# Optimization experiments

Measured on AMD Instinct MI355X. Metric: run time of the kernel, lower is better.

Reference implementation:

```python
import jax, jax.numpy as jnp
import numpy as np
import math

LOCAL_WINDOW = 256  # matches init_kwargs local_window

B, H, S, DK = 1, 16, 2048, 64


def setup_inputs() -> dict:
    key = jax.random.key(0)
    kq, kk, kv = jax.random.split(key, 3)
    return {
        "q": jax.random.normal(kq, (B, H, S, DK), dtype=jnp.float32),
        "k": jax.random.normal(kk, (B, H, S, DK), dtype=jnp.float32),
        "v": jax.random.normal(kv, (B, H, S, DK), dtype=jnp.float32),
        "layer_idx": 1,
        "training": 0,
    }


def _make_mask(seq_len: int, layer_idx: int) -> jnp.ndarray:
    i = jnp.arange(seq_len)[:, None]
    j = jnp.arange(seq_len)[None, :]
    causal = j <= i
    if layer_idx % 2 == 0:
        return causal  # full causal mask
    # local banded mask: causal AND within local_window
    return causal & ((i - j) < LOCAL_WINDOW)


def reference(q, k, v, layer_idx, training):
    # past=None path: no KV-cache concat; present = (k, v)
    dk = q.shape[-1]
    # scores: [B, H, S, S]
    scores = jnp.einsum("bhqd,bhkd->bhqk", q, k) / math.sqrt(dk)
    seq_len = scores.shape[-1]
    mask = _make_mask(seq_len, layer_idx)  # [S, S], broadcast over B, H
    scores = jnp.where(mask, scores, jnp.float32(-1e9))
    weights = jax.nn.softmax(scores, axis=-1)
    # training=0 -> no dropout (deterministic reference)
    context = jnp.einsum("bhqk,bhkd->bhqd", weights, v)
    return (context, k, v)  # (context, present)
```

## Files before the change

### kernel.cpp

```cpp
#include <hip/hip_runtime.h>

#define S_DIM 2048
#define H_DIM 16
#define DK_DIM 64
#define TQ 64
#define TK 64
#define KSP 72
#define VTP 72
#define PSP 72
#define WINDOW 256

typedef short short8 __attribute__((ext_vector_type(8)));
typedef float floatx4 __attribute__((ext_vector_type(4)));

static __device__ __forceinline__ short f2bf(float f) {
    unsigned u = __builtin_bit_cast(unsigned, f);
    u = (u + 0x7fffu + ((u >> 16) & 1u)) >> 16;
    return (short)u;
}

__global__ __launch_bounds__(256, 2)
void attn_kernel(const float* __restrict__ qg,
                 const float* __restrict__ kg,
                 const float* __restrict__ vg,
                 const int* __restrict__ layer_idx_p,
                 float* __restrict__ outc,
                 float* __restrict__ outk,
                 float* __restrict__ outv)
{
    __shared__ __align__(16) short Ks[TK * KSP];
    __shared__ __align__(16) short Vts[DK_DIM * VTP];
    __shared__ __align__(16) short Ps[4 * 16 * PSP];

    const int bid  = blockIdx.x;
    const int h    = bid >> 5;
    const int q0   = (bid & 31) * TQ;
    const int tid  = threadIdx.x;
    const int w    = tid >> 6;
    const int lane = tid & 63;
    const int quad = lane >> 4;
    const int l16  = lane & 15;

    const int li  = layer_idx_p[0];
    const int wnd = (li & 1) ? WINDOW : S_DIM;

    {
        const size_t base = ((size_t)(h * S_DIM + q0)) * DK_DIM;
        const floatx4* ks4 = (const floatx4*)(kg + base);
        const floatx4* vs4 = (const floatx4*)(vg + base);
        floatx4* ok4 = (floatx4*)(outk + base);
        floatx4* ov4 = (floatx4*)(outv + base);
        #pragma unroll
        for (int i = 0; i < 4; ++i) {
            int f = tid + i * 256;
            ok4[f] = ks4[f];
            ov4[f] = vs4[f];
        }
    }

    const int qrow = q0 + w * 16 + l16;
    const size_t qbase = ((size_t)(h * S_DIM + qrow)) * DK_DIM;
    short8 qf0, qf1;
    {
        floatx4 a0 = *(const floatx4*)(qg + qbase + quad * 8);
        floatx4 a1 = *(const floatx4*)(qg + qbase + quad * 8 + 4);
        floatx4 b0 = *(const floatx4*)(qg + qbase + 32 + quad * 8);
        floatx4 b1 = *(const floatx4*)(qg + qbase + 32 + quad * 8 + 4);
        #pragma unroll
        for (int j = 0; j < 4; ++j) {
            qf0[j]     = f2bf(a0[j] * 0.125f);
            qf0[j + 4] = f2bf(a1[j] * 0.125f);
            qf1[j]     = f2bf(b0[j] * 0.125f);
            qf1[j + 4] = f2bf(b1[j] * 0.125f);
        }
    }

    floatx4 Oacc[4];
    floatx4 Lacc = (floatx4){0.f, 0.f, 0.f, 0.f};
    #pragma unroll
    for (int dt = 0; dt < 4; ++dt) Oacc[dt] = (floatx4){0.f, 0.f, 0.f, 0.f};

    short8 ones;
    #pragma unroll
    for (int j = 0; j < 8; ++j) ones[j] = (short)0x3F80;

    int lo = q0 - (wnd - 1); if (lo < 0) lo = 0;
    const int kb0  = lo & ~(TK - 1);
    const int kend = q0 + TQ - 1;

    floatx4 kraw[2][2];
    float   vraw[2][8];
    const int krow[2] = { (tid * 8) >> 6, ((tid + 256) * 8) >> 6 };
    const int kcol[2] = { (tid * 8) & 63, ((tid + 256) * 8) & 63 };
    const int vd  [2] = { tid & 63, (tid + 256) & 63 };
    const int vkg [2] = { tid >> 6, (tid + 256) >> 6 };

    auto preload = [&](int kb) {
        #pragma unroll
        for (int it = 0; it < 2; ++it) {
            const float* p = kg + ((size_t)(h * S_DIM + kb + krow[it])) * DK_DIM + kcol[it];
            kraw[it][0] = *(const floatx4*)p;
            kraw[it][1] = *(const floatx4*)(p + 4);
            #pragma unroll
            for (int j = 0; j < 8; ++j)
                vraw[it][j] = vg[((size_t)(h * S_DIM + kb + vkg[it] * 8 + j)) * DK_DIM + vd[it]];
        }
    };
    auto commit = [&]() {
        #pragma unroll
        for (int it = 0; it < 2; ++it) {
            short8 val;
            #pragma unroll
            for (int j = 0; j < 4; ++j) {
                val[j]     = f2bf(kraw[it][0][j]);
                val[j + 4] = f2bf(kraw[it][1][j]);
            }
            *(short8*)(&Ks[krow[it] * KSP + kcol[it]]) = val;
            short8 tmp;
            #pragma unroll
            for (int j = 0; j < 8; ++j) tmp[j] = f2bf(vraw[it][j]);
            *(short8*)(&Vts[vd[it] * VTP + vkg[it] * 8]) = tmp;
        }
    };

    preload(kb0);

    for (int kb = kb0; kb <= kend; kb += TK) {
        commit();
        __syncthreads();
        if (kb + TK <= kend) preload(kb + TK);

        #pragma unroll
        for (int ct = 0; ct < 4; ++ct) {
            floatx4 acc = (floatx4){0.f, 0.f, 0.f, 0.f};
            short8 b0 = *(const short8*)(&Ks[(ct * 16 + l16) * KSP +      quad * 8]);
            acc = __builtin_amdgcn_mfma_f32_16x16x32_bf16(qf0, b0, acc, 0, 0, 0);
            short8 b1 = *(const short8*)(&Ks[(ct * 16 + l16) * KSP + 32 + quad * 8]);
            acc = __builtin_amdgcn_mfma_f32_16x16x32_bf16(qf1, b1, acc, 0, 0, 0);
            const int col = kb + ct * 16 + l16;
            #pragma unroll
            for (int r = 0; r < 4; ++r) {
                int row = q0 + w * 16 + quad * 4 + r;
                bool valid = (col <= row) && ((row - col) < wnd);
                float pv = valid ? __expf(acc[r]) : 0.f;
                Ps[(w * 16 + quad * 4 + r) * PSP + ct * 16 + l16] = f2bf(pv);
            }
        }

        #pragma unroll
        for (int ks = 0; ks < 2; ++ks) {
            short8 af = *(const short8*)(&Ps[(w * 16 + l16) * PSP + ks * 32 + quad * 8]);
            Lacc = __builtin_amdgcn_mfma_f32_16x16x32_bf16(af, ones, Lacc, 0, 0, 0);
            #pragma unroll
            for (int dt = 0; dt < 4; ++dt) {
                short8 bf = *(const short8*)(&Vts[(dt * 16 + l16) * VTP + ks * 32 + quad * 8]);
                Oacc[dt] = __builtin_amdgcn_mfma_f32_16x16x32_bf16(af, bf, Oacc[dt], 0, 0, 0);
            }
        }
        __syncthreads();
    }

    #pragma unroll
    for (int r = 0; r < 4; ++r) {
        float inv = 1.0f / Lacc[r];
        int row = q0 + w * 16 + quad * 4 + r;
        size_t obase = ((size_t)(h * S_DIM + row)) * DK_DIM;
        #pragma unroll
        for (int dt = 0; dt < 4; ++dt)
            outc[obase + dt * 16 + l16] = Oacc[dt][r] * inv;
    }
}

extern "C" void kernel_launch(void* const* d_in, const int* in_sizes, int n_in,
                              void* d_out, int out_size, void* d_ws, size_t ws_size,
                              hipStream_t stream) {
    const float* q  = (const float*)d_in[0];
    const float* k  = (const float*)d_in[1];
    const float* v  = (const float*)d_in[2];
    const int* li   = (const int*)d_in[3];
    float* out      = (float*)d_out;

    const int nctx = in_sizes[0];
    float* outk = out + nctx;
    float* outv = out + nctx + in_sizes[1];

    const int grid_attn = H_DIM * (S_DIM / TQ);
    attn_kernel<<<grid_attn, 256, 0, stream>>>(q, k, v, li, out, outk, outv);
}
```

Before: 97.29 us.

## Halve query tile and split key tiles across two wave groups

Measured after the change: 120.2 us. +23.6%, slower.

```diff
diff --git a/kernel.cpp b/kernel.cpp
--- a/kernel.cpp
+++ b/kernel.cpp
@@ -3,11 +3,9 @@
 #define S_DIM 2048
 #define H_DIM 16
 #define DK_DIM 64
-#define TQ 64
+#define TQ 32
 #define TK 64
-#define KSP 72
-#define VTP 72
-#define PSP 72
+#define PST 70
 #define WINDOW 256
 
 typedef short short8 __attribute__((ext_vector_type(8)));
@@ -19,7 +17,7 @@
     return (short)u;
 }
 
-__global__ __launch_bounds__(256, 2)
+__global__ __launch_bounds__(256, 3)
 void attn_kernel(const float* __restrict__ qg,
                  const float* __restrict__ kg,
                  const float* __restrict__ vg,
@@ -28,18 +26,21 @@
                  float* __restrict__ outk,
                  float* __restrict__ outv)
 {
-    __shared__ __align__(16) short Ks[TK * KSP];
-    __shared__ __align__(16) short Vts[DK_DIM * VTP];
-    __shared__ __align__(16) short Ps[4 * 16 * PSP];
+    __shared__ __align__(16) short Kst[2][TK * PST];
+    __shared__ __align__(16) short Vst[2][DK_DIM * PST];
+    __shared__ __align__(16) short Ps[4][16 * PST];
 
     const int bid  = blockIdx.x;
-    const int h    = bid >> 5;
-    const int q0   = (bid & 31) * TQ;
+    const int h    = bid >> 6;
+    const int q0   = (bid & 63) * TQ;
     const int tid  = threadIdx.x;
     const int w    = tid >> 6;
     const int lane = tid & 63;
     const int quad = lane >> 4;
     const int l16  = lane & 15;
+    const int qsub = w & 1;
+    const int kgrp = w >> 1;
+    const int t128 = tid & 127;
 
     const int li  = layer_idx_p[0];
     const int wnd = (li & 1) ? WINDOW : S_DIM;
@@ -51,14 +52,14 @@
         floatx4* ok4 = (floatx4*)(outk + base);
         floatx4* ov4 = (floatx4*)(outv + base);
         #pragma unroll
-        for (int i = 0; i < 4; ++i) {
+        for (int i = 0; i < 2; ++i) {
             int f = tid + i * 256;
             ok4[f] = ks4[f];
             ov4[f] = vs4[f];
         }
     }
 
-    const int qrow = q0 + w * 16 + l16;
+    const int qrow = q0 + qsub * 16 + l16;
     const size_t qbase = ((size_t)(h * S_DIM + qrow)) * DK_DIM;
     short8 qf0, qf1;
     {
@@ -85,89 +86,103 @@
     for (int j = 0; j < 8; ++j) ones[j] = (short)0x3F80;
 
     int lo = q0 - (wnd - 1); if (lo < 0) lo = 0;
-    const int kb0  = lo & ~(TK - 1);
-    const int kend = q0 + TQ - 1;
-
-    floatx4 kraw[2][2];
-    float   vraw[2][8];
-    const int krow[2] = { (tid * 8) >> 6, ((tid + 256) * 8) >> 6 };
-    const int kcol[2] = { (tid * 8) & 63, ((tid + 256) * 8) & 63 };
-    const int vd  [2] = { tid & 63, (tid + 256) & 63 };
-    const int vkg [2] = { tid >> 6, (tid + 256) >> 6 };
-
-    auto preload = [&](int kb) {
-        #pragma unroll
-        for (int it = 0; it < 2; ++it) {
-            const float* p = kg + ((size_t)(h * S_DIM + kb + krow[it])) * DK_DIM + kcol[it];
-            kraw[it][0] = *(const floatx4*)p;
-            kraw[it][1] = *(const floatx4*)(p + 4);
-            #pragma unroll
-            for (int j = 0; j < 8; ++j)
-                vraw[it][j] = vg[((size_t)(h * S_DIM + kb + vkg[it] * 8 + j)) * DK_DIM + vd[it]];
-        }
-    };
-    auto commit = [&]() {
-        #pragma unroll
-        for (int it = 0; it < 2; ++it) {
-            short8 val;
-            #pragma unroll
-            for (int j = 0; j < 4; ++j) {
-                val[j]     = f2bf(kraw[it][0][j]);
-                val[j + 4] = f2bf(kraw[it][1][j]);
-            }
-            *(short8*)(&Ks[krow[it] * KSP + kcol[it]]) = val;
-            short8 tmp;
-            #pragma unroll
-            for (int j = 0; j < 8; ++j) tmp[j] = f2bf(vraw[it][j]);
-            *(short8*)(&Vts[vd[it] * VTP + vkg[it] * 8]) = tmp;
-        }
-    };
-
-    preload(kb0);
-
-    for (int kb = kb0; kb <= kend; kb += TK) {
-        commit();
+    const int kb0 = lo & ~(TK - 1);
+    const int nc  = (q0 + TQ - kb0 + TK - 1) / TK;
+    const int na  = (nc + 1) >> 1;
+    const int myn = kgrp ? (nc - na) : na;
+    const int ofs = kgrp ? na : 0;
+
+    short* Kmy = Kst[kgrp];
+    short* Vmy = Vst[kgrp];
+    short* Pmy = Ps[w];
+
+    for (int i = 0; i < na; ++i) {
+        const bool act = (i < myn);
+        const int kb = kb0 + (ofs + i) * TK;
+
+        if (act) {
+            #pragma unroll
+            for (int it = 0; it < 4; ++it) {
+                int idx = t128 + it * 128;
+                int row = idx >> 3, col = (idx & 7) * 8;
+                const float* p = kg + ((size_t)(h * S_DIM + kb + row)) * DK_DIM + col;
+                floatx4 x0 = *(const floatx4*)p;
+                floatx4 x1 = *(const floatx4*)(p + 4);
+                short8 val;
+                #pragma unroll
+                for (int j = 0; j < 4; ++j) { val[j] = f2bf(x0[j]); val[j+4] = f2bf(x1[j]); }
+                *(short8*)(&Kmy[row * PST + col]) = val;
+            }
+            #pragma unroll
+            for (int it = 0; it < 4; ++it) {
+                int idx = t128 + it * 128;
+                int d = idx & 63, kg8 = idx >> 6;
+                short8 tmp;
+                #pragma unroll
+                for (int j = 0; j < 8; ++j)
+                    tmp[j] = f2bf(vg[((size_t)(h * S_DIM + kb + kg8 * 8 + j)) * DK_DIM + d]);
+                *(short8*)(&Vmy[d * PST + kg8 * 8]) = tmp;
+            }
+        }
         __syncthreads();
-        if (kb + TK <= kend) preload(kb + TK);
-
-        #pragma unroll
-        for (int ct = 0; ct < 4; ++ct) {
-            floatx4 acc = (floatx4){0.f, 0.f, 0.f, 0.f};
-            short8 b0 = *(const short8*)(&Ks[(ct * 16 + l16) * KSP +      quad * 8]);
-            acc = __builtin_amdgcn_mfma_f32_16x16x32_bf16(qf0, b0, acc, 0, 0, 0);
-            short8 b1 = *(const short8*)(&Ks[(ct * 16 + l16) * KSP + 32 + quad * 8]);
-            acc = __builtin_amdgcn_mfma_f32_16x16x32_bf16(qf1, b1, acc, 0, 0, 0);
-            const int col = kb + ct * 16 + l16;
-            #pragma unroll
-            for (int r = 0; r < 4; ++r) {
-                int row = q0 + w * 16 + quad * 4 + r;
-                bool valid = (col <= row) && ((row - col) < wnd);
-                float pv = valid ? __expf(acc[r]) : 0.f;
-                Ps[(w * 16 + quad * 4 + r) * PSP + ct * 16 + l16] = f2bf(pv);
-            }
-        }
-
-        #pragma unroll
-        for (int ks = 0; ks < 2; ++ks) {
-            short8 af = *(const short8*)(&Ps[(w * 16 + l16) * PSP + ks * 32 + quad * 8]);
-            Lacc = __builtin_amdgcn_mfma_f32_16x16x32_bf16(af, ones, Lacc, 0, 0, 0);
+
+        if (act) {
+            #pragma unroll
+            for (int ct = 0; ct < 4; ++ct) {
+                floatx4 acc = (floatx4){0.f, 0.f, 0.f, 0.f};
+                short8 b0 = *(const short8*)(&Kmy[(ct * 16 + l16) * PST +      quad * 8]);
+                acc = __builtin_amdgcn_mfma_f32_16x16x32_bf16(qf0, b0, acc, 0, 0, 0);
+                short8 b1 = *(const short8*)(&Kmy[(ct * 16 + l16) * PST + 32 + quad * 8]);
+                acc = __builtin_amdgcn_mfma_f32_16x16x32_bf16(qf1, b1, acc, 0, 0, 0);
+                const int col = kb + ct * 16 + l16;
+                #pragma unroll
+                for (int r = 0; r < 4; ++r) {
+                    int row = q0 + qsub * 16 + quad * 4 + r;
+                    bool valid = (col <= row) && ((row - col) < wnd);
+                    float pv = valid ? __expf(acc[r]) : 0.f;
+                    Pmy[(quad * 4 + r) * PST + ct * 16 + l16] = f2bf(pv);
+                }
+            }
+            #pragma unroll
+            for (int ks = 0; ks < 2; ++ks) {
+                short8 af = *(const short8*)(&Pmy[l16 * PST + ks * 32 + quad * 8]);
+                Lacc = __builtin_amdgcn_mfma_f32_16x16x32_bf16(af, ones, Lacc, 0, 0, 0);
+                #pragma unroll
+                for (int dt = 0; dt < 4; ++dt) {
+                    short8 bf = *(const short8*)(&Vmy[(dt * 16 + l16) * PST + ks * 32 + quad * 8]);
+                    Oacc[dt] = __builtin_amdgcn_mfma_f32_16x16x32_bf16(af, bf, Oacc[dt], 0, 0, 0);
+                }
+            }
+        }
+        __syncthreads();
+    }
+
+    float* scr = (float*)(qsub ? Vst[1] : Kst[1]);
+    if (kgrp == 1) {
+        #pragma unroll
+        for (int dt = 0; dt < 4; ++dt)
+            #pragma unroll
+            for (int r = 0; r < 4; ++r)
+                scr[(quad * 4 + r) * 64 + dt * 16 + l16] = Oacc[dt][r];
+        if (l16 == 0)
+            #pragma unroll
+            for (int r = 0; r < 4; ++r)
+                scr[1024 + quad * 4 + r] = Lacc[r];
+    }
+    __syncthreads();
+    if (kgrp == 0) {
+        #pragma unroll
+        for (int r = 0; r < 4; ++r) {
+            float l = Lacc[r] + scr[1024 + quad * 4 + r];
+            float inv = 1.0f / l;
+            int row = q0 + qsub * 16 + quad * 4 + r;
+            size_t obase = ((size_t)(h * S_DIM + row)) * DK_DIM;
             #pragma unroll
             for (int dt = 0; dt < 4; ++dt) {
-                short8 bf = *(const short8*)(&Vts[(dt * 16 + l16) * VTP + ks * 32 + quad * 8]);
-                Oacc[dt] = __builtin_amdgcn_mfma_f32_16x16x32_bf16(af, bf, Oacc[dt], 0, 0, 0);
-            }
-        }
-        __syncthreads();
-    }
-
-    #pragma unroll
-    for (int r = 0; r < 4; ++r) {
-        float inv = 1.0f / Lacc[r];
-        int row = q0 + w * 16 + quad * 4 + r;
-        size_t obase = ((size_t)(h * S_DIM + row)) * DK_DIM;
-        #pragma unroll
-        for (int dt = 0; dt < 4; ++dt)
-            outc[obase + dt * 16 + l16] = Oacc[dt][r] * inv;
+                float o = Oacc[dt][r] + scr[(quad * 4 + r) * 64 + dt * 16 + l16];
+                outc[obase + dt * 16 + l16] = o * inv;
+            }
+        }
     }
 }
 
```
